# Performance work log

Measured on AMD Instinct MI355X. Metric: run time of the kernel, lower is better.

The kernel has to match this reference:

```python
import jax, jax.numpy as jnp
import numpy as np

L1 = 512
LX = 32
COUNT = 8


def setup_inputs() -> dict:
    key = jax.random.key(0)
    ks = jax.random.split(key, 9)
    B = 65536
    x = jax.random.uniform(ks[0], (B, 2 * L1), dtype=jnp.float32)  # NNUE accumulator is in [0,1]
    ls_indices = jax.random.randint(ks[1], (B,), 0, COUNT, dtype=jnp.int64)
    # params (scaled ~1/sqrt(fan_in))
    w_fact = jax.random.normal(ks[2], (LX, 2 * L1), dtype=jnp.float32) * (1.0 / np.sqrt(2 * L1))
    w0 = jax.random.normal(ks[3], (LX * COUNT, 2 * L1), dtype=jnp.float32) * (1.0 / np.sqrt(2 * L1))
    b0 = jax.random.normal(ks[4], (LX * COUNT,), dtype=jnp.float32) * 0.05
    w1 = jax.random.normal(ks[5], (LX * COUNT, LX), dtype=jnp.float32) * (1.0 / np.sqrt(LX))
    b1 = jax.random.normal(ks[6], (LX * COUNT,), dtype=jnp.float32) * 0.05
    w2 = jax.random.normal(ks[7], (1 * COUNT, LX), dtype=jnp.float32) * (1.0 / np.sqrt(LX))
    b2 = jax.random.normal(ks[8], (1 * COUNT,), dtype=jnp.float32) * 0.05
    return {"x": x, "ls_indices": ls_indices, "w_fact": w_fact,
            "w0": w0, "b0": b0, "w1": w1, "b1": b1, "w2": w2, "b2": b2}


def _stack_linear_gather(h, w, b, idx, out_dim):
    # dense Linear for all COUNT buckets, then gather the selected bucket per row
    y = (h @ w.T + b).reshape(-1, COUNT, out_dim)          # [B, COUNT, out_dim]
    return y.reshape(-1, out_dim)[idx]                      # [B, out_dim]


def reference(x, ls_indices, w_fact, w0, b0, w1, b1, w2, b2):
    B = x.shape[0]
    idx = ls_indices.astype(jnp.int32) + jnp.arange(B, dtype=jnp.int32) * COUNT
    l1f = x @ w_fact.T                                      # [B, LX]
    h = _stack_linear_gather(x, w0, b0, idx, LX) + l1f      # layer 0 + factorized term
    h = jnp.clip(h, 0.0, 1.0)
    h = _stack_linear_gather(h, w1, b1, idx, LX)            # hidden layer 1
    h = jnp.clip(h, 0.0, 1.0)
    out = _stack_linear_gather(h, w2, b2, idx, 1)           # output layer (no clamp)
    return out
```

## Files before the change

### kernel.cpp

```cpp
#include <hip/hip_runtime.h>


#define B_ROWS 65536
#define LK     1024
#define TILE   128
#define NCHUNK 16
#define MAIN_BLOCKS (B_ROWS / TILE + 8)

#define SORTED_OFF 1024
#define WB_OFF     (1024 + 131072)

typedef short  short8  __attribute__((ext_vector_type(8)));
typedef float  f32x16  __attribute__((ext_vector_type(16)));

__device__ __forceinline__ unsigned pkbf(float a, float b) {
    unsigned ua = __float_as_uint(a), ub = __float_as_uint(b);
    ua = (ua + 0x7FFFu + ((ua >> 16) & 1u)) >> 16;
    ub = (ub + 0x7FFFu + ((ub >> 16) & 1u)) >> 16;
    return (ua & 0xFFFFu) | (ub << 16);
}

__device__ __forceinline__ bool detect_i64(const int* p) {
    int acc = 0;
#pragma unroll
    for (int i = 0; i < 64; ++i) acc |= p[2 * i + 1];
    return acc == 0;
}

__device__ __forceinline__ int load_bucket(const int* p, int r, bool i64) {
    return (i64 ? p[2 * r] : p[r]) & 7;
}

__global__ __launch_bounds__(1024) void k_prep(
    const int* __restrict__ idx, const float* __restrict__ w0,
    const float* __restrict__ wf, uint4* __restrict__ wB,
    unsigned short* __restrict__ sorted, int* __restrict__ hdr)
{
    int t = threadIdx.x;

    if (blockIdx.x > 0) {
        int f = (blockIdx.x - 1) * 1024 + t;
        int b   = f >> 12;
        int kc  = (f >> 8) & 15;
        int i8  = f & 255;
        int n   = i8 & 31;
        int khi = i8 >> 5;
        int k = kc * 64 + khi * 8;
        const float* p0 = w0 + (size_t)(b * 32 + n) * LK + k;
        const float* pf = wf + (size_t)n * LK + k;
        float v[8];
#pragma unroll
        for (int j = 0; j < 8; ++j) v[j] = p0[j] + pf[j];
        uint4 o;
        o.x = pkbf(v[0], v[1]); o.y = pkbf(v[2], v[3]);
        o.z = pkbf(v[4], v[5]); o.w = pkbf(v[6], v[7]);
        wB[f] = o;
        return;
    }

    __shared__ int wcnt[16][8];
    __shared__ int wbase[16][8];
    __shared__ int segb[8];

    bool i64 = detect_i64(idx);
    int wv = t >> 6, lane = t & 63;
    int rowbase = wv * 4096;

    int mycnt = 0;
    for (int i = 0; i < 64; ++i) {
        int r = rowbase + i * 64 + lane;
        int b = load_bucket(idx, r, i64);
#pragma unroll
        for (int bb = 0; bb < 8; ++bb) {
            unsigned long long m = __ballot(b == bb);
            if (lane == bb) mycnt += __popcll(m);
        }
    }
    if (lane < 8) wcnt[wv][lane] = mycnt;
    __syncthreads();

    if (t == 0) {
        int base = 0, tt = 0;
        for (int b = 0; b < 8; ++b) {
            int tot = 0;
            for (int w = 0; w < 16; ++w) tot += wcnt[w][b];
            hdr[b] = tot; hdr[16 + b] = base; hdr[24 + b] = tt;
            segb[b] = base;
            base += tot;
            tt += (tot + TILE - 1) / TILE;
        }
        hdr[24 + 8] = tt;
    }
    __syncthreads();

    if (t < 128) {
        int w2 = t >> 3, b = t & 7;
        int base = segb[b];
        for (int w = 0; w < w2; ++w) base += wcnt[w][b];
        wbase[w2][b] = base;
    }
    __syncthreads();

    int mycur = (lane < 8) ? wbase[wv][lane] : 0;
    for (int i = 0; i < 64; ++i) {
        int r = rowbase + i * 64 + lane;
        int b = load_bucket(idx, r, i64);
        unsigned long long mown = 0;
        int addc = 0;
#pragma unroll
        for (int bb = 0; bb < 8; ++bb) {
            unsigned long long m = __ballot(b == bb);
            if (b == bb) mown = m;
            if (lane == bb) addc = __popcll(m);
        }
        int base = __shfl(mycur, b);
        int rank = __popcll(mown & ((1ull << lane) - 1ull));
        sorted[base + rank] = (unsigned short)r;
        mycur += addc;
    }
}

__global__ __launch_bounds__(256, 4) void k_main(
    const float* __restrict__ x, const unsigned short* __restrict__ sorted,
    const int* __restrict__ hdr, const uint4* __restrict__ wB,
    const float* __restrict__ b0, const float* __restrict__ w1,
    const float* __restrict__ b1, const float* __restrict__ w2,
    const float* __restrict__ b2, float* __restrict__ out)
{
    __shared__ __align__(16) unsigned char smem[32768];
    uint4* Abuf = (uint4*)smem;
    float* hbuf = (float*)smem;

    int total = hdr[24 + 8];
    int g = blockIdx.x;
    if (g >= total) return;

    int bkt = 0;
    while (bkt < 7 && hdr[24 + bkt + 1] <= g) bkt++;
    int tile  = g - hdr[24 + bkt];
    int cnt   = hdr[bkt];
    int seg   = hdr[16 + bkt];
    int p0    = seg + tile * TILE;
    int nrows = min(TILE, cnt - tile * TILE);

    int t    = threadIdx.x;
    int lane = t & 63;
    int wv   = t >> 6;

    int khi = t >> 5;
    const float* xrow[4];
#pragma unroll
    for (int it = 0; it < 4; ++it) {
        int rloc = (t & 31) + 32 * it;
        int rc = min(rloc, nrows - 1);
        int gr = (int)sorted[p0 + rc];
        xrow[it] = x + (size_t)gr * LK + khi * 8;
    }
    const short8* wBg = (const short8*)(wB + (size_t)bkt * 4096);

    float4 pfa[8];
    auto loadA = [&](int kc) {
#pragma unroll
        for (int it = 0; it < 4; ++it) {
            const float4* p = (const float4*)(xrow[it] + kc * 64);
            pfa[2 * it]     = p[0];
            pfa[2 * it + 1] = p[1];
        }
    };
    auto storeA = [&](int buf) {
#pragma unroll
        for (int it = 0; it < 4; ++it) {
            float4 a = pfa[2 * it], c = pfa[2 * it + 1];
            uint4 o;
            o.x = pkbf(a.x, a.y); o.y = pkbf(a.z, a.w);
            o.z = pkbf(c.x, c.y); o.w = pkbf(c.z, c.w);
            Abuf[buf * 1024 + 256 * it + t] = o;
        }
    };

    f32x16 acc;
#pragma unroll
    for (int i = 0; i < 16; ++i) acc[i] = 0.0f;

    loadA(0);
    storeA(0);
    __syncthreads();

    for (int kc = 0; kc < NCHUNK; ++kc) {
        int cur = kc & 1;
        short8 bfr[4];
#pragma unroll
        for (int kk = 0; kk < 4; ++kk) bfr[kk] = wBg[kc * 256 + kk * 64 + lane];
        if (kc < NCHUNK - 1) loadA(kc + 1);
        const short8* Af = (const short8*)&Abuf[cur * 1024 + 256 * wv];
#pragma unroll
        for (int kk = 0; kk < 4; ++kk) {
            short8 av = Af[lane + 64 * kk];
            acc = __builtin_amdgcn_mfma_f32_32x32x16_bf16(av, bfr[kk], acc, 0, 0, 0);
        }
        if (kc < NCHUNK - 1) storeA(cur ^ 1);
        __syncthreads();
    }

    int jl = lane & 31;
    float b0v = b0[bkt * 32 + jl];
#pragma unroll
    for (int reg = 0; reg < 16; ++reg) {
        int rowl = 32 * wv + (reg & 3) + 8 * (reg >> 2) + 4 * (lane >> 5);
        float h = acc[reg] + b0v;
        h = fminf(fmaxf(h, 0.0f), 1.0f);
        hbuf[rowl * 36 + jl] = h;
    }
    __syncthreads();

    int r = t >> 1, half = t & 1;
    const float4* hr = (const float4*)&hbuf[r * 36];
    float4 ha[8];
#pragma unroll
    for (int q = 0; q < 8; ++q) ha[q] = hr[q];
    const float* w1b = w1 + (size_t)bkt * 1024;
    const float* b1b = b1 + bkt * 32;
    const float* w2b = w2 + bkt * 32;
    float partial = 0.0f;
#pragma unroll
    for (int jj = 0; jj < 16; ++jj) {
        int j2 = half * 16 + jj;
        const float4* wr = (const float4*)&w1b[j2 * 32];
        float s = b1b[j2];
#pragma unroll
        for (int q = 0; q < 8; ++q) {
            float4 w4 = wr[q];
            s += ha[q].x * w4.x + ha[q].y * w4.y + ha[q].z * w4.z + ha[q].w * w4.w;
        }
        s = fminf(fmaxf(s, 0.0f), 1.0f);
        partial += s * w2b[j2];
    }
    partial += __shfl_xor(partial, 1);
    if (half == 0 && r < nrows) {
        int gr = (int)sorted[p0 + r];
        out[gr] = partial + b2[bkt];
    }
}

extern "C" void kernel_launch(void* const* d_in, const int* in_sizes, int n_in,
                              void* d_out, int out_size, void* d_ws, size_t ws_size,
                              hipStream_t stream) {
    const float* x   = (const float*)d_in[0];
    const int*   lsi = (const int*)  d_in[1];
    const float* wf  = (const float*)d_in[2];
    const float* w0  = (const float*)d_in[3];
    const float* b0  = (const float*)d_in[4];
    const float* w1  = (const float*)d_in[5];
    const float* b1  = (const float*)d_in[6];
    const float* w2  = (const float*)d_in[7];
    const float* b2  = (const float*)d_in[8];
    float* out = (float*)d_out;

    char* ws = (char*)d_ws;
    int* hdr = (int*)ws;
    unsigned short* sorted = (unsigned short*)(ws + SORTED_OFF);
    uint4* wB = (uint4*)(ws + WB_OFF);

    k_prep<<<33, 1024, 0, stream>>>(lsi, w0, wf, wB, sorted, hdr);
    k_main<<<MAIN_BLOCKS, 256, 0, stream>>>(x, sorted, hdr, wB,
                                            b0, w1, b1, w2, b2, out);
}
```

Measured before the change: 486.4 us.

## Use 32-row tiles with whole-row staging and split-K across waves

```diff
diff --git a/kernel.cpp b/kernel.cpp
--- a/kernel.cpp
+++ b/kernel.cpp
@@ -3,9 +3,9 @@
 
 #define B_ROWS 65536
 #define LK     1024
-#define TILE   128
-#define NCHUNK 16
+#define TILE   32
 #define MAIN_BLOCKS (B_ROWS / TILE + 8)
+#define SROW   2056
 
 #define SORTED_OFF 1024
 #define WB_OFF     (1024 + 131072)
@@ -41,8 +41,9 @@
     if (blockIdx.x > 0) {
         int f = (blockIdx.x - 1) * 1024 + t;
         int b   = f >> 12;
-        int kc  = (f >> 8) & 15;
-        int i8  = f & 255;
+        int i12 = f & 4095;
+        int kc  = i12 >> 8;
+        int i8  = i12 & 255;
         int n   = i8 & 31;
         int khi = i8 >> 5;
         int k = kc * 64 + khi * 8;
@@ -66,17 +67,23 @@
     int wv = t >> 6, lane = t & 63;
     int rowbase = wv * 4096;
 
-    int mycnt = 0;
+    unsigned nib[8] = {0, 0, 0, 0, 0, 0, 0, 0};
+    int c[8] = {0, 0, 0, 0, 0, 0, 0, 0};
+#pragma unroll 8
     for (int i = 0; i < 64; ++i) {
         int r = rowbase + i * 64 + lane;
         int b = load_bucket(idx, r, i64);
-#pragma unroll
-        for (int bb = 0; bb < 8; ++bb) {
-            unsigned long long m = __ballot(b == bb);
-            if (lane == bb) mycnt += __popcll(m);
-        }
-    }
-    if (lane < 8) wcnt[wv][lane] = mycnt;
+        nib[i >> 3] |= (unsigned)b << (4 * (i & 7));
+#pragma unroll
+        for (int bb = 0; bb < 8; ++bb) c[bb] += (b == bb) ? 1 : 0;
+    }
+#pragma unroll
+    for (int bb = 0; bb < 8; ++bb) {
+        int v = c[bb];
+#pragma unroll
+        for (int s = 1; s < 64; s <<= 1) v += __shfl_xor(v, s);
+        if (lane == 0) wcnt[wv][bb] = v;
+    }
     __syncthreads();
 
     if (t == 0) {
@@ -102,9 +109,9 @@
     __syncthreads();
 
     int mycur = (lane < 8) ? wbase[wv][lane] : 0;
+#pragma unroll
     for (int i = 0; i < 64; ++i) {
-        int r = rowbase + i * 64 + lane;
-        int b = load_bucket(idx, r, i64);
+        int b = (nib[i >> 3] >> (4 * (i & 7))) & 7;
         unsigned long long mown = 0;
         int addc = 0;
 #pragma unroll
@@ -115,21 +122,21 @@
         }
         int base = __shfl(mycur, b);
         int rank = __popcll(mown & ((1ull << lane) - 1ull));
-        sorted[base + rank] = (unsigned short)r;
+        sorted[base + rank] = (unsigned short)(rowbase + i * 64 + lane);
         mycur += addc;
     }
 }
 
-__global__ __launch_bounds__(256, 4) void k_main(
+__global__ __launch_bounds__(256, 2) void k_main(
     const float* __restrict__ x, const unsigned short* __restrict__ sorted,
     const int* __restrict__ hdr, const uint4* __restrict__ wB,
     const float* __restrict__ b0, const float* __restrict__ w1,
     const float* __restrict__ b1, const float* __restrict__ w2,
     const float* __restrict__ b2, float* __restrict__ out)
 {
-    __shared__ __align__(16) unsigned char smem[32768];
-    uint4* Abuf = (uint4*)smem;
-    float* hbuf = (float*)smem;
+    __shared__ __align__(16) unsigned char smem[TILE * SROW];
+    float* rbuf = (float*)smem;
+    float* hb   = (float*)(smem + 16384);
 
     int total = hdr[24 + 8];
     int g = blockIdx.x;
@@ -147,98 +154,93 @@
     int lane = t & 63;
     int wv   = t >> 6;
 
-    int khi = t >> 5;
-    const float* xrow[4];
-#pragma unroll
-    for (int it = 0; it < 4; ++it) {
-        int rloc = (t & 31) + 32 * it;
-        int rc = min(rloc, nrows - 1);
-        int gr = (int)sorted[p0 + rc];
-        xrow[it] = x + (size_t)gr * LK + khi * 8;
-    }
-    const short8* wBg = (const short8*)(wB + (size_t)bkt * 4096);
-
-    float4 pfa[8];
-    auto loadA = [&](int kc) {
-#pragma unroll
-        for (int it = 0; it < 4; ++it) {
-            const float4* p = (const float4*)(xrow[it] + kc * 64);
-            pfa[2 * it]     = p[0];
-            pfa[2 * it + 1] = p[1];
-        }
-    };
-    auto storeA = [&](int buf) {
-#pragma unroll
-        for (int it = 0; it < 4; ++it) {
-            float4 a = pfa[2 * it], c = pfa[2 * it + 1];
-            uint4 o;
-            o.x = pkbf(a.x, a.y); o.y = pkbf(a.z, a.w);
-            o.z = pkbf(c.x, c.y); o.w = pkbf(c.z, c.w);
-            Abuf[buf * 1024 + 256 * it + t] = o;
-        }
-    };
+#pragma unroll
+    for (int j0 = 0; j0 < 32; j0 += 8) {
+        float4 v[8];
+#pragma unroll
+        for (int jj = 0; jj < 8; ++jj) {
+            int j = j0 + jj;
+            int gr = (int)sorted[p0 + min(j, nrows - 1)];
+            v[jj] = ((const float4*)(x + (size_t)gr * LK))[t];
+        }
+#pragma unroll
+        for (int jj = 0; jj < 8; ++jj) {
+            int j = j0 + jj;
+            uint2 o;
+            o.x = pkbf(v[jj].x, v[jj].y);
+            o.y = pkbf(v[jj].z, v[jj].w);
+            *(uint2*)(smem + j * SROW + t * 8) = o;
+        }
+    }
+    __syncthreads();
+
+    const uint4* wBg = wB + (size_t)bkt * 4096;
+    const unsigned char* Abase = smem + (size_t)(lane & 31) * SROW + 16 * (lane >> 5);
 
     f32x16 acc;
 #pragma unroll
     for (int i = 0; i < 16; ++i) acc[i] = 0.0f;
 
-    loadA(0);
-    storeA(0);
-    __syncthreads();
-
-    for (int kc = 0; kc < NCHUNK; ++kc) {
-        int cur = kc & 1;
-        short8 bfr[4];
-#pragma unroll
-        for (int kk = 0; kk < 4; ++kk) bfr[kk] = wBg[kc * 256 + kk * 64 + lane];
-        if (kc < NCHUNK - 1) loadA(kc + 1);
-        const short8* Af = (const short8*)&Abuf[cur * 1024 + 256 * wv];
-#pragma unroll
-        for (int kk = 0; kk < 4; ++kk) {
-            short8 av = Af[lane + 64 * kk];
-            acc = __builtin_amdgcn_mfma_f32_32x32x16_bf16(av, bfr[kk], acc, 0, 0, 0);
-        }
-        if (kc < NCHUNK - 1) storeA(cur ^ 1);
-        __syncthreads();
-    }
-
-    int jl = lane & 31;
-    float b0v = b0[bkt * 32 + jl];
-#pragma unroll
-    for (int reg = 0; reg < 16; ++reg) {
-        int rowl = 32 * wv + (reg & 3) + 8 * (reg >> 2) + 4 * (lane >> 5);
-        float h = acc[reg] + b0v;
+    union UA { uint2 h[2]; short8 s; };
+    union UB { uint4 u;    short8 s; };
+#pragma unroll
+    for (int cc = 0; cc < 16; ++cc) {
+        int c = wv * 16 + cc;
+        UA ua;
+        ua.h[0] = *(const uint2*)(Abase + 32 * c);
+        ua.h[1] = *(const uint2*)(Abase + 32 * c + 8);
+        UB ub;
+        ub.u = wBg[c * 64 + lane];
+        acc = __builtin_amdgcn_mfma_f32_32x32x16_bf16(ua.s, ub.s, acc, 0, 0, 0);
+    }
+
+    __syncthreads();
+#pragma unroll
+    for (int r = 0; r < 16; ++r)
+        rbuf[wv * 1024 + r * 64 + lane] = acc[r];
+    __syncthreads();
+
+#pragma unroll
+    for (int q = 0; q < 4; ++q) {
+        int e = t + 256 * q;
+        float s = rbuf[e] + rbuf[1024 + e] + rbuf[2048 + e] + rbuf[3072 + e];
+        int rr = e >> 6, ll = e & 63;
+        int m = (rr & 3) + 8 * (rr >> 2) + 4 * (ll >> 5);
+        int n = ll & 31;
+        float h = s + b0[bkt * 32 + n];
         h = fminf(fmaxf(h, 0.0f), 1.0f);
-        hbuf[rowl * 36 + jl] = h;
-    }
-    __syncthreads();
-
-    int r = t >> 1, half = t & 1;
-    const float4* hr = (const float4*)&hbuf[r * 36];
-    float4 ha[8];
-#pragma unroll
-    for (int q = 0; q < 8; ++q) ha[q] = hr[q];
-    const float* w1b = w1 + (size_t)bkt * 1024;
-    const float* b1b = b1 + bkt * 32;
-    const float* w2b = w2 + bkt * 32;
-    float partial = 0.0f;
-#pragma unroll
-    for (int jj = 0; jj < 16; ++jj) {
-        int j2 = half * 16 + jj;
-        const float4* wr = (const float4*)&w1b[j2 * 32];
-        float s = b1b[j2];
-#pragma unroll
-        for (int q = 0; q < 8; ++q) {
-            float4 w4 = wr[q];
-            s += ha[q].x * w4.x + ha[q].y * w4.y + ha[q].z * w4.z + ha[q].w * w4.w;
-        }
-        s = fminf(fmaxf(s, 0.0f), 1.0f);
-        partial += s * w2b[j2];
-    }
-    partial += __shfl_xor(partial, 1);
-    if (half == 0 && r < nrows) {
-        int gr = (int)sorted[p0 + r];
-        out[gr] = partial + b2[bkt];
+        hb[m * 36 + n] = h;
+    }
+    __syncthreads();
+
+    if (t < 64) {
+        int r = t >> 1, half = t & 1;
+        const float4* hr = (const float4*)(hb + r * 36);
+        float4 ha[8];
+#pragma unroll
+        for (int q = 0; q < 8; ++q) ha[q] = hr[q];
+        const float* w1b = w1 + (size_t)bkt * 1024;
+        const float* b1b = b1 + bkt * 32;
+        const float* w2b = w2 + bkt * 32;
+        float partial = 0.0f;
+#pragma unroll
+        for (int jj = 0; jj < 16; ++jj) {
+            int j2 = half * 16 + jj;
+            const float4* wr = (const float4*)&w1b[j2 * 32];
+            float s = b1b[j2];
+#pragma unroll
+            for (int q = 0; q < 8; ++q) {
+                float4 w4 = wr[q];
+                s += ha[q].x * w4.x + ha[q].y * w4.y + ha[q].z * w4.z + ha[q].w * w4.w;
+            }
+            s = fminf(fmaxf(s, 0.0f), 1.0f);
+            partial += s * w2b[j2];
+        }
+        partial += __shfl_xor(partial, 1);
+        if (half == 0 && r < nrows) {
+            int gr = (int)sorted[p0 + r];
+            out[gr] = partial + b2[bkt];
+        }
     }
 }
 
```

Result: faster. 434.3 us (-10.7%).
